# Performance work log

Measured on AMD Instinct MI355X. Metric: run time of the kernel, lower is better.

The kernel has to match this reference:

```python
import jax, jax.numpy as jnp
import numpy as np

D_MODEL = 2048
H_TOTAL = 32
D_HEAD = D_MODEL // H_TOTAL  # 64
H_ACTIVE = 4
ROPE_BASE = 10000.0


def _apply_rope(t, cos, sin):
    # t: [B, H, T, DH]; cos/sin: [T, DH//2]; interleaved pair rotation
    t1 = t[..., 0::2]
    t2 = t[..., 1::2]
    r1 = t1 * cos - t2 * sin
    r2 = t1 * sin + t2 * cos
    return jnp.stack([r1, r2], axis=-1).reshape(t.shape)


def setup_inputs() -> dict:
    key = jax.random.key(0)
    ks = jax.random.split(key, 4)
    x = jax.random.normal(ks[0], (4, 1024, D_MODEL), dtype=jnp.float32)
    w_router = jax.random.normal(ks[1], (D_MODEL, H_TOTAL), dtype=jnp.float32) * 0.02
    w_qkv = jax.random.normal(ks[2], (D_MODEL, 3 * D_MODEL), dtype=jnp.float32) * 0.02
    w_out = jax.random.normal(ks[3], (D_MODEL, D_MODEL), dtype=jnp.float32) * 0.02
    return {"x": x, "w_router": w_router, "w_qkv": w_qkv, "w_out": w_out}


def reference(x, w_router, w_qkv, w_out):
    B, T, _ = x.shape
    # --- SwitchRouter: per-token probabilities over heads ---
    probs = jax.nn.softmax(x @ w_router, axis=-1)            # [B, T, H]
    # top-h_active heads per token (dense-math equivalent of sparse dispatch)
    _, top_idx = jax.lax.top_k(probs, H_ACTIVE)              # [B, T, HA]
    mask = jnp.sum(jax.nn.one_hot(top_idx, H_TOTAL, dtype=x.dtype), axis=-2)  # [B, T, H]
    gate = probs * mask                                      # router-scored gate

    # --- QKV projection ---
    qkv = x @ w_qkv                                          # [B, T, 3D]
    q, k, v = jnp.split(qkv, 3, axis=-1)
    def to_heads(t):
        return t.reshape(B, T, H_TOTAL, D_HEAD).transpose(0, 2, 1, 3)  # [B, H, T, DH]
    q, k, v = to_heads(q), to_heads(k), to_heads(v)

    # --- RoPE ---
    inv_freq = 1.0 / (ROPE_BASE ** (jnp.arange(0, D_HEAD, 2, dtype=jnp.float32) / D_HEAD))
    ang = jnp.arange(T, dtype=jnp.float32)[:, None] * inv_freq[None, :]  # [T, DH/2]
    cos, sin = jnp.cos(ang), jnp.sin(ang)
    q = _apply_rope(q, cos, sin)
    k = _apply_rope(k, cos, sin)

    # --- causal SDPA ---
    scores = jnp.einsum('bhqd,bhkd->bhqk', q, k) / np.float32(np.sqrt(D_HEAD))
    causal = jnp.tril(jnp.ones((T, T), dtype=bool))
    scores = jnp.where(causal, scores, jnp.finfo(scores.dtype).min)
    attn = jax.nn.softmax(scores, axis=-1)
    out = jnp.einsum('bhqk,bhkd->bhqd', attn, v)             # [B, H, T, DH]

    # --- gate: only active heads contribute (scatter-back equivalent) ---
    out = out * gate.transpose(0, 2, 1)[..., None]           # [B, H, T, DH]
    out = out.transpose(0, 2, 1, 3).reshape(B, T, D_MODEL)
    return out @ w_out
```

## Files before the change

### kernel.cpp

```cpp
#include <hip/hip_runtime.h>
#include <hip/hip_bf16.h>
#include <stdint.h>
#include <stddef.h>

typedef __attribute__((ext_vector_type(8))) short bf16x8;
typedef __attribute__((ext_vector_type(8))) unsigned short u16x8;
typedef __attribute__((ext_vector_type(4))) float f32x4;
typedef __attribute__((ext_vector_type(16))) float f32x16;

#define TT 1024

__device__ __forceinline__ unsigned short f2bf(float f){
  unsigned u = __builtin_bit_cast(unsigned, f);
  unsigned r = 0x7fffu + ((u >> 16) & 1u);
  return (unsigned short)((u + r) >> 16);
}
__device__ __forceinline__ float bf2f(unsigned short s){
  unsigned u = ((unsigned)s) << 16;
  return __builtin_bit_cast(float, u);
}
__device__ __forceinline__ void gload16(const unsigned short* g, unsigned short* l){
  __builtin_amdgcn_global_load_lds(
      (const __attribute__((address_space(1))) void*)g,
      (__attribute__((address_space(3))) void*)l, 16, 0, 0);
}

#define MFMA32(a, b, c) __builtin_amdgcn_mfma_f32_32x32x16_bf16((a), (b), (c), 0, 0, 0)
#define MFMA_B16(a, b, c) __builtin_amdgcn_mfma_f32_16x16x32_bf16((a), (b), (c), 0, 0, 0)

__global__ void transpose_w_kernel(const float* __restrict__ wqkv, const float* __restrict__ wout,
                                   unsigned short* __restrict__ wqkvT, unsigned short* __restrict__ woutT){
  __shared__ float tile[32][33];
  const float* in; unsigned short* out; int C;
  int bx = blockIdx.x;
  if (bx < 192){ in = wqkv; out = wqkvT; C = 6144; }
  else         { in = wout; out = woutT; C = 2048; bx -= 192; }
  const int R = 2048;
  int c0 = bx * 32, r0 = blockIdx.y * 32;
  for (int i = threadIdx.y; i < 32; i += 8)
    tile[i][threadIdx.x] = in[(size_t)(r0 + i) * C + c0 + threadIdx.x];
  __syncthreads();
  for (int i = threadIdx.y; i < 32; i += 8)
    out[(size_t)(c0 + i) * R + r0 + threadIdx.x] = f2bf(tile[threadIdx.x][i]);
}

__global__ __launch_bounds__(256) void prep_kernel(const float* __restrict__ x,
                                                   const float* __restrict__ wr,
                                                   unsigned short* __restrict__ x_bf,
                                                   float* __restrict__ gate,
                                                   unsigned char* __restrict__ heads4,
                                                   float* __restrict__ tab){
  __shared__ float xc[8 * 256];
  __shared__ float red[8 * 8 * 32];
  const int tid = threadIdx.x;
  const int tok0 = blockIdx.x * 8;
  const int p = tid >> 5, h = tid & 31;

  if (blockIdx.x < 128){
    int i2 = blockIdx.x * 256 + tid;
    int pos = i2 >> 5, ii = i2 & 31;
    float freq = powf(10000.0f, -(float)ii / 32.0f);
    float ang = (float)pos * freq;
    tab[i2 * 2]     = cosf(ang);
    tab[i2 * 2 + 1] = sinf(ang);
  }

  float acc[8] = {0.f,0.f,0.f,0.f,0.f,0.f,0.f,0.f};
  for (int kb = 0; kb < 8; kb++){
    __syncthreads();
    {
      int tok = tid >> 5, e = (tid & 31) * 8;
      const float* xp = x + (size_t)(tok0 + tok) * 2048 + kb * 256 + e;
      float4 v0 = *(const float4*)xp, v1 = *(const float4*)(xp + 4);
      float vals[8] = {v0.x, v0.y, v0.z, v0.w, v1.x, v1.y, v1.z, v1.w};
      u16x8 ob;
      #pragma unroll
      for (int jj = 0; jj < 8; jj++) ob[jj] = f2bf(vals[jj]);
      *(u16x8*)(x_bf + (size_t)(tok0 + tok) * 2048 + kb * 256 + e) = ob;
      #pragma unroll
      for (int jj = 0; jj < 8; jj++) xc[tok * 256 + e + jj] = vals[jj];
    }
    __syncthreads();
    const float* wp = wr + (size_t)(kb * 256 + p * 32) * 32 + h;
    #pragma unroll 4
    for (int j = 0; j < 32; j++){
      float wv = wp[j * 32];
      #pragma unroll
      for (int tok = 0; tok < 8; tok++)
        acc[tok] += xc[tok * 256 + p * 32 + j] * wv;
    }
  }
  #pragma unroll
  for (int tok = 0; tok < 8; tok++) red[(p * 8 + tok) * 32 + h] = acc[tok];
  __syncthreads();
  {
    int lane = tid & 63;
    int tok = (tid >> 6) * 2 + (lane >> 5);
    int hh = lane & 31;
    float logit = 0.f;
    #pragma unroll
    for (int pp = 0; pp < 8; pp++) logit += red[(pp * 8 + tok) * 32 + hh];
    float m = logit;
    #pragma unroll
    for (int s = 16; s >= 1; s >>= 1) m = fmaxf(m, __shfl_xor(m, s));
    float e = __expf(logit - m);
    float sum = e;
    #pragma unroll
    for (int s = 16; s >= 1; s >>= 1) sum += __shfl_xor(sum, s);
    float prob = e / sum;
    float v = logit; int sel = 0;
    #pragma unroll
    for (int rr2 = 0; rr2 < 4; rr2++){
      float bv = v; int bi = hh;
      #pragma unroll
      for (int s = 16; s >= 1; s >>= 1){
        float ov = __shfl_xor(bv, s); int oi = __shfl_xor(bi, s);
        if (ov > bv || (ov == bv && oi < bi)) { bv = ov; bi = oi; }
      }
      if (hh == bi) { sel = 1; v = -3.4e38f; }
    }
    gate[(size_t)(tok0 + tok) * 32 + hh] = sel ? prob : 0.f;
    unsigned long long bal = __ballot(sel != 0);
    unsigned selmask = (unsigned)(bal >> ((lane >> 5) * 32));
    if (sel){
      int r = __popc(selmask & ((1u << hh) - 1u));
      heads4[(size_t)(tok0 + tok) * 4 + r] = (unsigned char)hh;
    }
  }
}

__global__ void compact_kernel(const unsigned char* __restrict__ heads4,
                               unsigned short* __restrict__ idx, int* __restrict__ counts){
  int bh = blockIdx.x;
  int b = bh >> 5, h = bh & 31;
  int lane = threadIdx.x;
  int base = 0;
  for (int c = 0; c < 16; c++){
    int t = c * 64 + lane;
    unsigned u = ((const unsigned*)heads4)[b * 1024 + t];
    int r = -1;
    if (((u      ) & 255) == (unsigned)h) r = 0;
    else if (((u >>  8) & 255) == (unsigned)h) r = 1;
    else if (((u >> 16) & 255) == (unsigned)h) r = 2;
    else if (((u >> 24) & 255) == (unsigned)h) r = 3;
    bool act = (r >= 0);
    unsigned long long mask = __ballot(act);
    int pos = base + __popcll(mask & ((1ull << lane) - 1ull));
    if (act) idx[bh * 1024 + pos] = (unsigned short)(t | (r << 10));
    base += __popcll(mask);
  }
  if (lane == 0) counts[bh] = base;
}

template<int MREP, int EPI>
__global__ __launch_bounds__(256, 2) void gemmk(const unsigned short* __restrict__ A,
                                                const unsigned short* __restrict__ Bt,
                                                float* __restrict__ Cf,
                                                unsigned short* __restrict__ kbuf,
                                                unsigned short* __restrict__ vt,
                                                const float* __restrict__ tab,
                                                int N, int K, int nbm){
  extern __shared__ unsigned short smem[];
  constexpr int BM = MREP * 64;
  constexpr int AU = MREP * 2048;
  constexpr int SLOT = AU + 4096;
  const int nblk = gridDim.x;
  const int raw = blockIdx.x;
  const int tile = (raw & 7) * (nblk >> 3) + (raw >> 3);
  const int bn = tile / nbm, bm = tile % nbm;

  const int tid = threadIdx.x, lane = tid & 63, wid = tid >> 6;
  const int wrow = wid >> 1, wcol = wid & 1;
  const int l31 = lane & 31, hi = lane >> 5;
  const int X = ((l31 >> 1) & 7) << 4;

  const unsigned short* gA[MREP];
  const unsigned short* gB[2];
  #pragma unroll
  for (int p = 0; p < MREP; p++){
    int L = tid * 16 + p * 4096;
    int line = L >> 7;
    int cs = (L & 127) ^ ((line & 7) << 4);
    gA[p] = A + (size_t)(bm * BM + line * 2 + (cs >> 6)) * K + ((cs & 63) >> 1);
  }
  #pragma unroll
  for (int p = 0; p < 2; p++){
    int L = tid * 16 + p * 4096;
    int line = L >> 7;
    int cs = (L & 127) ^ ((line & 7) << 4);
    gB[p] = Bt + (size_t)(bn * 128 + line * 2 + (cs >> 6)) * K + ((cs & 63) >> 1);
  }

  f32x16 acc[MREP][2];
  #pragma unroll
  for (int i = 0; i < MREP; i++)
    #pragma unroll
    for (int j = 0; j < 2; j++) acc[i][j] = f32x16{0,0,0,0,0,0,0,0,0,0,0,0,0,0,0,0};

  const int NT = K >> 5;
  #pragma unroll
  for (int tt = 0; tt < 2; tt++){
    unsigned short* sb = smem + tt * SLOT;
    #pragma unroll
    for (int p = 0; p < MREP; p++) gload16(gA[p] + (size_t)tt * 32, sb + tid * 8 + p * 2048);
    #pragma unroll
    for (int p = 0; p < 2; p++)    gload16(gB[p] + (size_t)tt * 32, sb + AU + tid * 8 + p * 2048);
  }

  for (int t = 0; t < NT; ++t){
    if (t < NT - 1){
      if constexpr (MREP == 4) asm volatile("s_waitcnt vmcnt(6)" ::: "memory");
      else                     asm volatile("s_waitcnt vmcnt(4)" ::: "memory");
    } else                     asm volatile("s_waitcnt vmcnt(0)" ::: "memory");
    __builtin_amdgcn_s_barrier();
    __builtin_amdgcn_sched_barrier(0);
    const unsigned short* bs = smem + (t % 3) * SLOT;
    unsigned short* ns = smem + ((t + 2) % 3) * SLOT;
    const bool st = (t + 2 < NT);
    #pragma unroll
    for (int ks = 0; ks < 2; ks++){
      const int bo = (((l31 & 1) * 64 + ks * 32 + hi * 16) ^ X) >> 1;
      bf16x8 av[MREP], bv[2];
      #pragma unroll
      for (int i = 0; i < MREP; i++)
        av[i] = *(const bf16x8*)(bs + (wrow * (MREP * 16) + i * 16 + (l31 >> 1)) * 64 + bo);
      #pragma unroll
      for (int j = 0; j < 2; j++)
        bv[j] = *(const bf16x8*)(bs + AU + (wcol * 32 + j * 16 + (l31 >> 1)) * 64 + bo);
      if (st){
        if (ks == 0){
          #pragma unroll
          for (int p = 0; p < MREP / 2 + 1; p++)
            gload16(gA[p] + (size_t)(t + 2) * 32, ns + tid * 8 + p * 2048);
        } else {
          #pragma unroll
          for (int p = MREP / 2 + 1; p < MREP; p++)
            gload16(gA[p] + (size_t)(t + 2) * 32, ns + tid * 8 + p * 2048);
          #pragma unroll
          for (int p = 0; p < 2; p++)
            gload16(gB[p] + (size_t)(t + 2) * 32, ns + AU + tid * 8 + p * 2048);
        }
      }
      #pragma unroll
      for (int i = 0; i < MREP; i++){
        acc[i][0] = MFMA32(av[i], bv[0], acc[i][0]);
        acc[i][1] = MFMA32(av[i], bv[1], acc[i][1]);
      }
    }
  }

  if constexpr (EPI == 1){
    if (bn < 16){
      #pragma unroll
      for (int i = 0; i < MREP; i++){
        #pragma unroll
        for (int j = 0; j < 2; j++){
          int col = bn * 128 + wcol * 64 + j * 32 + l31;
          int ii = (col & 63) >> 1;
          #pragma unroll
          for (int g = 0; g < 4; g++){
            #pragma unroll
            for (int rr = 0; rr < 4; rr++){
              int row = bm * BM + wrow * (BM / 2) + i * 32 + g * 8 + hi * 4 + rr;
              int pos = row & (TT - 1);
              const float* tp = tab + ((size_t)pos * 32 + ii) * 2;
              float c = tp[0], s = tp[1];
              float val = acc[i][j][g * 4 + rr];
              float pv = __shfl_xor(val, 1);
              float res = (lane & 1) ? (pv * s + val * c) : (val * c - pv * s);
              kbuf[(size_t)row * 2048 + col] = f2bf(res);
            }
          }
        }
      }
    } else {
      #pragma unroll
      for (int i = 0; i < MREP; i++){
        #pragma unroll
        for (int j = 0; j < 2; j++){
          int vcol = bn * 128 + wcol * 64 + j * 32 + l31 - 2048;
          int hh = vcol >> 6, d = vcol & 63;
          int row0 = bm * BM + wrow * (BM / 2) + i * 32 + hi * 4;
          int b = row0 >> 10, t0 = row0 & (TT - 1);
          #pragma unroll
          for (int g = 0; g < 4; g++){
            ushort4 pk;
            pk.x = f2bf(acc[i][j][g * 4 + 0]); pk.y = f2bf(acc[i][j][g * 4 + 1]);
            pk.z = f2bf(acc[i][j][g * 4 + 2]); pk.w = f2bf(acc[i][j][g * 4 + 3]);
            *(ushort4*)(vt + ((size_t)((b * 32 + hh) * 64 + d)) * TT + t0 + g * 8) = pk;
          }
        }
      }
    }
  } else {
    #pragma unroll
    for (int i = 0; i < MREP; i++){
      #pragma unroll
      for (int j = 0; j < 2; j++){
        int col = bn * 128 + wcol * 64 + j * 32 + l31;
        #pragma unroll
        for (int g = 0; g < 4; g++){
          #pragma unroll
          for (int rr = 0; rr < 4; rr++){
            size_t row = (size_t)(bm * BM + wrow * (BM / 2) + i * 32 + g * 8 + hi * 4 + rr);
            Cf[row * N + col] = acc[i][j][g * 4 + rr];
          }
        }
      }
    }
  }
}

__global__ __launch_bounds__(256) void attn_fused(const unsigned short* __restrict__ x_bf,
                                                  const unsigned short* __restrict__ wqkvT,
                                                  const unsigned short* __restrict__ kbuf,
                                                  const unsigned short* __restrict__ vt,
                                                  const float* __restrict__ gate,
                                                  const unsigned short* __restrict__ idx,
                                                  const int* __restrict__ counts,
                                                  const float* __restrict__ tab,
                                                  unsigned short* __restrict__ attn_out){
  __shared__ unsigned short Ks[64 * 64];
  __shared__ unsigned short Vs[64 * 64];
  __shared__ unsigned short Ps[4][16 * 64];
  __shared__ unsigned short Qb[4][16 * 64];
  const int bh = blockIdx.x, qt = blockIdx.y;
  const int count = counts[bh];
  if (qt * 64 >= count) return;
  const int b = bh >> 5, h = bh & 31;
  const int tid = threadIdx.x, lane = tid & 63, w = tid >> 6;
  const int li = lane & 15, lg = lane >> 4;
  const unsigned short* myidx = idx + bh * 1024 + qt * 64;
  const int nvalid = min(64, count - qt * 64);
  const int qmax = myidx[nvalid - 1] & 1023;

  int qi[4];
  #pragma unroll
  for (int r = 0; r < 4; r++){
    int s = w * 16 + lg * 4 + r;
    qi[r] = (s < nvalid) ? (myidx[s] & 1023) : -1;
  }

  {
    int s = w * 16 + li;
    int tokA = (s < nvalid) ? (myidx[s] & 1023) : 0;
    const unsigned short* xrow = x_bf + (size_t)(b * 1024 + tokA) * 2048;
    const unsigned short* wq = wqkvT + (size_t)(h * 64) * 2048;
    f32x4 qa[4];
    #pragma unroll
    for (int ni = 0; ni < 4; ni++) qa[ni] = f32x4{0.f, 0.f, 0.f, 0.f};
    #pragma unroll 2
    for (int kk = 0; kk < 64; kk++){
      int k0 = kk * 32 + lg * 8;
      bf16x8 af = *(const bf16x8*)(xrow + k0);
      #pragma unroll
      for (int ni = 0; ni < 4; ni++){
        bf16x8 bw = *(const bf16x8*)(wq + (size_t)(ni * 16 + li) * 2048 + k0);
        qa[ni] = MFMA_B16(af, bw, qa[ni]);
      }
    }
    #pragma unroll
    for (int ni = 0; ni < 4; ni++){
      int col = ni * 16 + li;
      #pragma unroll
      for (int r = 0; r < 4; r++){
        int tq = (qi[r] < 0) ? 0 : qi[r];
        const float* tp = tab + ((size_t)tq * 32 + (col >> 1)) * 2;
        float c = tp[0], sn = tp[1];
        float val = qa[ni][r];
        float pv = __shfl_xor(val, 1);
        float res = (li & 1) ? (pv * sn + val * c) : (val * c - pv * sn);
        int row = lg * 4 + r;
        Qb[w][(row * 128 + ((col * 2) ^ ((row & 7) << 4))) >> 1] = f2bf(res * 0.125f);
      }
    }
  }
  const int kX = (li & 7) << 4;
  bf16x8 qf0 = *(const bf16x8*)(&Qb[w][(li * 128 + ((lg * 16) ^ kX)) >> 1]);
  bf16x8 qf1 = *(const bf16x8*)(&Qb[w][(li * 128 + ((64 + lg * 16) ^ kX)) >> 1]);

  f32x4 o[4];
  #pragma unroll
  for (int i = 0; i < 4; i++) o[i] = f32x4{0.f, 0.f, 0.f, 0.f};
  float m_run[4], l_run[4];
  #pragma unroll
  for (int r = 0; r < 4; r++){ m_run[r] = -1e30f; l_run[r] = 0.f; }

  const int nkt = (qmax >> 6) + 1;
  for (int kt = 0; kt < nkt; kt++){
    const int kb = kt * 64;
    #pragma unroll
    for (int s2 = 0; s2 < 2; s2++){
      int ss = s2 * 256 + tid;
      int r = ss >> 3;
      int ce = (((ss & 7) * 16) ^ ((r & 7) << 4)) >> 1;
      gload16(kbuf + (size_t)(b * TT + kb + r) * 2048 + h * 64 + ce, &Ks[ss * 8]);
      gload16(vt + (size_t)(bh * 64 + r) * TT + kb + ce, &Vs[ss * 8]);
    }
    __syncthreads();

    f32x4 s4[4];
    #pragma unroll
    for (int ni = 0; ni < 4; ni++){
      int rb = (ni * 16 + li) * 128;
      bf16x8 k0 = *(const bf16x8*)(&Ks[(rb + ((lg * 16) ^ kX)) >> 1]);
      bf16x8 k1 = *(const bf16x8*)(&Ks[(rb + ((64 + lg * 16) ^ kX)) >> 1]);
      f32x4 t = f32x4{0.f, 0.f, 0.f, 0.f};
      t = MFMA_B16(qf0, k0, t);
      t = MFMA_B16(qf1, k1, t);
      s4[ni] = t;
    }
    float mt[4];
    #pragma unroll
    for (int r = 0; r < 4; r++) mt[r] = -1e30f;
    #pragma unroll
    for (int ni = 0; ni < 4; ni++){
      int kidx = kb + ni * 16 + li;
      #pragma unroll
      for (int r = 0; r < 4; r++){
        float val = s4[ni][r];
        val = (kidx <= qi[r]) ? val : -1e30f;
        s4[ni][r] = val;
        mt[r] = fmaxf(mt[r], val);
      }
    }
    #pragma unroll
    for (int r = 0; r < 4; r++){
      #pragma unroll
      for (int sh = 8; sh >= 1; sh >>= 1) mt[r] = fmaxf(mt[r], __shfl_xor(mt[r], sh));
      float mnew = fmaxf(m_run[r], mt[r]);
      float corr = __expf(m_run[r] - mnew);
      m_run[r] = mnew;
      l_run[r] *= corr;
      #pragma unroll
      for (int j = 0; j < 4; j++) o[j][r] *= corr;
    }
    float rs[4] = {0.f, 0.f, 0.f, 0.f};
    #pragma unroll
    for (int ni = 0; ni < 4; ni++)
      #pragma unroll
      for (int r = 0; r < 4; r++){
        float p = __expf(s4[ni][r] - m_run[r]);
        s4[ni][r] = p;
        rs[r] += p;
      }
    #pragma unroll
    for (int r = 0; r < 4; r++){
      #pragma unroll
      for (int sh = 8; sh >= 1; sh >>= 1) rs[r] += __shfl_xor(rs[r], sh);
      l_run[r] += rs[r];
    }
    #pragma unroll
    for (int ni = 0; ni < 4; ni++)
      #pragma unroll
      for (int r = 0; r < 4; r++){
        int row = lg * 4 + r;
        Ps[w][(row * 128 + (((ni * 16 + li) * 2) ^ ((row & 7) << 4))) >> 1] = f2bf(s4[ni][r]);
      }
    #pragma unroll
    for (int ks = 0; ks < 2; ks++){
      bf16x8 pa = *(const bf16x8*)(&Ps[w][(li * 128 + ((ks * 64 + lg * 16) ^ kX)) >> 1]);
      #pragma unroll
      for (int ni = 0; ni < 4; ni++){
        bf16x8 vb = *(const bf16x8*)(&Vs[((ni * 16 + li) * 128 + ((ks * 64 + lg * 16) ^ kX)) >> 1]);
        o[ni] = MFMA_B16(pa, vb, o[ni]);
      }
    }
    __syncthreads();
  }
  #pragma unroll
  for (int r = 0; r < 4; r++){
    if (qi[r] < 0) continue;
    float g = gate[(size_t)(b * TT + qi[r]) * 32 + h];
    float inv = g / l_run[r];
    #pragma unroll
    for (int ni = 0; ni < 4; ni++)
      attn_out[(size_t)(b * TT + qi[r]) * 2048 + h * 64 + ni * 16 + li] = f2bf(o[ni][r] * inv);
  }
}

extern "C" void kernel_launch(void* const* d_in, const int* in_sizes, int n_in,
                              void* d_out, int out_size, void* d_ws, size_t ws_size,
                              hipStream_t stream){
  const float* x        = (const float*)d_in[0];
  const float* w_router = (const float*)d_in[1];
  const float* w_qkv    = (const float*)d_in[2];
  const float* w_out    = (const float*)d_in[3];
  float* out = (float*)d_out;
  char* ws = (char*)d_ws;

  unsigned short* kbuf   = (unsigned short*)(ws);
  unsigned short* vt     = (unsigned short*)(ws + 16777216);
  unsigned short* idx    = (unsigned short*)(ws + 37748736);
  int* counts            = (int*)(ws + 38010880);
  unsigned char* heads4  = (unsigned char*)(ws + 38011392);
  unsigned short* x_bf   = (unsigned short*)(ws + 50331648);
  unsigned short* wqkvT  = (unsigned short*)(ws + 67108864);
  unsigned short* woutT  = (unsigned short*)(ws + 92274688);
  float* gate            = (float*)(ws + 100663296);
  float* tab             = (float*)(ws + 101187584);
  unsigned short* attn   = (unsigned short*)(ws + 67108864 + 8388608);

  constexpr int KV_LDS  = 3 * (4 * 4096 + 8192);
  constexpr int OUT_LDS = 3 * (2 * 4096 + 8192);
  (void)hipFuncSetAttribute(reinterpret_cast<const void*>(&gemmk<4, 1>),
                            hipFuncAttributeMaxDynamicSharedMemorySize, KV_LDS);
  (void)hipFuncSetAttribute(reinterpret_cast<const void*>(&gemmk<2, 0>),
                            hipFuncAttributeMaxDynamicSharedMemorySize, OUT_LDS);

  hipLaunchKernelGGL(transpose_w_kernel, dim3(256, 64), dim3(32, 8), 0, stream, w_qkv, w_out, wqkvT, woutT);
  hipLaunchKernelGGL(prep_kernel, dim3(512), dim3(256), 0, stream, x, w_router, x_bf, gate, heads4, tab);
  hipLaunchKernelGGL(compact_kernel, dim3(128), dim3(64), 0, stream, heads4, idx, counts);
  hipLaunchKernelGGL((gemmk<4, 1>), dim3(512), dim3(256), KV_LDS, stream,
                     x_bf, wqkvT + (size_t)2048 * 2048, (float*)nullptr, kbuf, vt, tab, 4096, 2048, 16);
  (void)hipMemsetAsync(attn, 0, (size_t)4096 * 2048 * 2, stream);
  hipLaunchKernelGGL(attn_fused, dim3(128, 16), dim3(256), 0, stream,
                     x_bf, wqkvT, kbuf, vt, gate, idx, counts, tab, attn);
  hipLaunchKernelGGL((gemmk<2, 0>), dim3(512), dim3(256), OUT_LDS, stream,
                     attn, woutT, out, (unsigned short*)nullptr, (unsigned short*)nullptr,
                     (const float*)nullptr, 2048, 2048, 32);
}
```

Before: 297.8 us.

## Split sparse Q projection into separate split-K GEMM kernel before attention

Moves the per-token Q projection and RoPE out of the attention kernel into a dedicated qgemm kernel. That kernel computes a 64-token by 64-dim tile per block, splits K across four waves, reduces the partial sums in LDS and writes RoPE'd bf16 Q into a compact per-(token, slot) buffer. The attention kernel then just loads Q fragments, applies the 1/8 scale to the scores, and drops the XOR swizzle on its K, V and P LDS tiles, which may add bank conflicts. The attention output buffer now reuses the x_bf region. This adds a kernel launch and a global round trip for Q, in exchange for better MFMA reuse in the projection.

```diff
diff --git a/kernel.cpp b/kernel.cpp
--- a/kernel.cpp
+++ b/kernel.cpp
@@ -150,6 +150,80 @@
     base += __popcll(mask);
   }
   if (lane == 0) counts[bh] = base;
+}
+
+__global__ __launch_bounds__(256) void qgemm_kernel(const unsigned short* __restrict__ x_bf,
+                                                    const unsigned short* __restrict__ wqkvT,
+                                                    const unsigned short* __restrict__ idx,
+                                                    const int* __restrict__ counts,
+                                                    const float* __restrict__ tab,
+                                                    unsigned short* __restrict__ qact){
+  __shared__ float red[4][64][64];
+  const int bh = blockIdx.x, qt = blockIdx.y;
+  const int count = counts[bh];
+  if (qt * 64 >= count) return;
+  const int b = bh >> 5, h = bh & 31;
+  const int tid = threadIdx.x, lane = tid & 63, w = tid >> 6;
+  const int li = lane & 15, lg = lane >> 4;
+  const int nvalid = min(64, count - qt * 64);
+  const unsigned short* myidx = idx + bh * 1024 + qt * 64;
+
+  int atok[4];
+  #pragma unroll
+  for (int ai = 0; ai < 4; ai++){
+    int s = ai * 16 + li;
+    atok[ai] = (s < nvalid) ? (myidx[s] & 1023) : 0;
+  }
+  const unsigned short* Bbase = wqkvT + (size_t)(h * 64) * 2048;
+
+  f32x4 acc[4][4];
+  #pragma unroll
+  for (int i = 0; i < 4; i++)
+    #pragma unroll
+    for (int j = 0; j < 4; j++) acc[i][j] = f32x4{0.f, 0.f, 0.f, 0.f};
+
+  const int k0w = w * 512;
+  #pragma unroll 2
+  for (int ks = 0; ks < 16; ks++){
+    int k0 = k0w + ks * 32 + lg * 8;
+    bf16x8 af[4], bw[4];
+    #pragma unroll
+    for (int ai = 0; ai < 4; ai++)
+      af[ai] = *(const bf16x8*)(x_bf + (size_t)(b * 1024 + atok[ai]) * 2048 + k0);
+    #pragma unroll
+    for (int ni = 0; ni < 4; ni++)
+      bw[ni] = *(const bf16x8*)(Bbase + (size_t)(ni * 16 + li) * 2048 + k0);
+    #pragma unroll
+    for (int ai = 0; ai < 4; ai++)
+      #pragma unroll
+      for (int ni = 0; ni < 4; ni++)
+        acc[ai][ni] = MFMA_B16(af[ai], bw[ni], acc[ai][ni]);
+  }
+  #pragma unroll
+  for (int ai = 0; ai < 4; ai++)
+    #pragma unroll
+    for (int ni = 0; ni < 4; ni++)
+      #pragma unroll
+      for (int rr = 0; rr < 4; rr++)
+        red[w][ai * 16 + lg * 4 + rr][ni * 16 + li] = acc[ai][ni][rr];
+  __syncthreads();
+
+  int q = tid >> 2, dbase = (tid & 3) * 16;
+  if (q < nvalid){
+    int e = myidx[q];
+    int tok = e & 1023, r = e >> 10;
+    unsigned short* op = qact + ((size_t)((b << 10) + tok) * 4 + r) * 64;
+    const float* tp = tab + ((size_t)tok * 32 + (dbase >> 1)) * 2;
+    #pragma unroll
+    for (int p = 0; p < 8; p++){
+      int d0 = dbase + 2 * p;
+      float v0 = red[0][q][d0] + red[1][q][d0] + red[2][q][d0] + red[3][q][d0];
+      float v1 = red[0][q][d0 + 1] + red[1][q][d0 + 1] + red[2][q][d0 + 1] + red[3][q][d0 + 1];
+      float c = tp[2 * p], s = tp[2 * p + 1];
+      op[d0]     = f2bf(v0 * c - v1 * s);
+      op[d0 + 1] = f2bf(v0 * s + v1 * c);
+    }
+  }
 }
 
 template<int MREP, int EPI>
@@ -311,19 +385,16 @@
   }
 }
 
-__global__ __launch_bounds__(256) void attn_fused(const unsigned short* __restrict__ x_bf,
-                                                  const unsigned short* __restrict__ wqkvT,
-                                                  const unsigned short* __restrict__ kbuf,
-                                                  const unsigned short* __restrict__ vt,
-                                                  const float* __restrict__ gate,
-                                                  const unsigned short* __restrict__ idx,
-                                                  const int* __restrict__ counts,
-                                                  const float* __restrict__ tab,
-                                                  unsigned short* __restrict__ attn_out){
+__global__ __launch_bounds__(256) void attn_sparse_kernel(const unsigned short* __restrict__ qact,
+                                                          const unsigned short* __restrict__ kbuf,
+                                                          const unsigned short* __restrict__ vt,
+                                                          const float* __restrict__ gate,
+                                                          const unsigned short* __restrict__ idx,
+                                                          const int* __restrict__ counts,
+                                                          unsigned short* __restrict__ attn_out){
   __shared__ unsigned short Ks[64 * 64];
   __shared__ unsigned short Vs[64 * 64];
   __shared__ unsigned short Ps[4][16 * 64];
-  __shared__ unsigned short Qb[4][16 * 64];
   const int bh = blockIdx.x, qt = blockIdx.y;
   const int count = counts[bh];
   if (qt * 64 >= count) return;
@@ -340,45 +411,14 @@
     int s = w * 16 + lg * 4 + r;
     qi[r] = (s < nvalid) ? (myidx[s] & 1023) : -1;
   }
-
+  bf16x8 qf0, qf1;
   {
     int s = w * 16 + li;
-    int tokA = (s < nvalid) ? (myidx[s] & 1023) : 0;
-    const unsigned short* xrow = x_bf + (size_t)(b * 1024 + tokA) * 2048;
-    const unsigned short* wq = wqkvT + (size_t)(h * 64) * 2048;
-    f32x4 qa[4];
-    #pragma unroll
-    for (int ni = 0; ni < 4; ni++) qa[ni] = f32x4{0.f, 0.f, 0.f, 0.f};
-    #pragma unroll 2
-    for (int kk = 0; kk < 64; kk++){
-      int k0 = kk * 32 + lg * 8;
-      bf16x8 af = *(const bf16x8*)(xrow + k0);
-      #pragma unroll
-      for (int ni = 0; ni < 4; ni++){
-        bf16x8 bw = *(const bf16x8*)(wq + (size_t)(ni * 16 + li) * 2048 + k0);
-        qa[ni] = MFMA_B16(af, bw, qa[ni]);
-      }
-    }
-    #pragma unroll
-    for (int ni = 0; ni < 4; ni++){
-      int col = ni * 16 + li;
-      #pragma unroll
-      for (int r = 0; r < 4; r++){
-        int tq = (qi[r] < 0) ? 0 : qi[r];
-        const float* tp = tab + ((size_t)tq * 32 + (col >> 1)) * 2;
-        float c = tp[0], sn = tp[1];
-        float val = qa[ni][r];
-        float pv = __shfl_xor(val, 1);
-        float res = (li & 1) ? (pv * sn + val * c) : (val * c - pv * sn);
-        int row = lg * 4 + r;
-        Qb[w][(row * 128 + ((col * 2) ^ ((row & 7) << 4))) >> 1] = f2bf(res * 0.125f);
-      }
-    }
-  }
-  const int kX = (li & 7) << 4;
-  bf16x8 qf0 = *(const bf16x8*)(&Qb[w][(li * 128 + ((lg * 16) ^ kX)) >> 1]);
-  bf16x8 qf1 = *(const bf16x8*)(&Qb[w][(li * 128 + ((64 + lg * 16) ^ kX)) >> 1]);
-
+    int e2 = (s < nvalid) ? myidx[s] : 0;
+    const unsigned short* qp = qact + ((size_t)((b << 10) + (e2 & 1023)) * 4 + (e2 >> 10)) * 64;
+    qf0 = *(const bf16x8*)(qp + lg * 8);
+    qf1 = *(const bf16x8*)(qp + 32 + lg * 8);
+  }
   f32x4 o[4];
   #pragma unroll
   for (int i = 0; i < 4; i++) o[i] = f32x4{0.f, 0.f, 0.f, 0.f};
@@ -391,20 +431,18 @@
     const int kb = kt * 64;
     #pragma unroll
     for (int s2 = 0; s2 < 2; s2++){
-      int ss = s2 * 256 + tid;
-      int r = ss >> 3;
-      int ce = (((ss & 7) * 16) ^ ((r & 7) << 4)) >> 1;
-      gload16(kbuf + (size_t)(b * TT + kb + r) * 2048 + h * 64 + ce, &Ks[ss * 8]);
-      gload16(vt + (size_t)(bh * 64 + r) * TT + kb + ce, &Vs[ss * 8]);
+      int s = s2 * 256 + tid;
+      int r = s >> 3, c = (s & 7) * 8;
+      gload16(kbuf + (size_t)(b * TT + kb + r) * 2048 + h * 64 + c, &Ks[s * 8]);
+      gload16(vt + (size_t)(bh * 64 + r) * TT + kb + c, &Vs[s * 8]);
     }
     __syncthreads();
 
     f32x4 s4[4];
     #pragma unroll
     for (int ni = 0; ni < 4; ni++){
-      int rb = (ni * 16 + li) * 128;
-      bf16x8 k0 = *(const bf16x8*)(&Ks[(rb + ((lg * 16) ^ kX)) >> 1]);
-      bf16x8 k1 = *(const bf16x8*)(&Ks[(rb + ((64 + lg * 16) ^ kX)) >> 1]);
+      bf16x8 k0 = *(const bf16x8*)(&Ks[(ni * 16 + li) * 64 + lg * 8]);
+      bf16x8 k1 = *(const bf16x8*)(&Ks[(ni * 16 + li) * 64 + 32 + lg * 8]);
       f32x4 t = f32x4{0.f, 0.f, 0.f, 0.f};
       t = MFMA_B16(qf0, k0, t);
       t = MFMA_B16(qf1, k1, t);
@@ -418,7 +456,7 @@
       int kidx = kb + ni * 16 + li;
       #pragma unroll
       for (int r = 0; r < 4; r++){
-        float val = s4[ni][r];
+        float val = s4[ni][r] * 0.125f;
         val = (kidx <= qi[r]) ? val : -1e30f;
         s4[ni][r] = val;
         mt[r] = fmaxf(mt[r], val);
@@ -453,16 +491,14 @@
     #pragma unroll
     for (int ni = 0; ni < 4; ni++)
       #pragma unroll
-      for (int r = 0; r < 4; r++){
-        int row = lg * 4 + r;
-        Ps[w][(row * 128 + (((ni * 16 + li) * 2) ^ ((row & 7) << 4))) >> 1] = f2bf(s4[ni][r]);
-      }
+      for (int r = 0; r < 4; r++)
+        Ps[w][(lg * 4 + r) * 64 + ni * 16 + li] = f2bf(s4[ni][r]);
     #pragma unroll
     for (int ks = 0; ks < 2; ks++){
-      bf16x8 pa = *(const bf16x8*)(&Ps[w][(li * 128 + ((ks * 64 + lg * 16) ^ kX)) >> 1]);
+      bf16x8 pa = *(const bf16x8*)(&Ps[w][li * 64 + ks * 32 + lg * 8]);
       #pragma unroll
       for (int ni = 0; ni < 4; ni++){
-        bf16x8 vb = *(const bf16x8*)(&Vs[((ni * 16 + li) * 128 + ((ks * 64 + lg * 16) ^ kX)) >> 1]);
+        bf16x8 vb = *(const bf16x8*)(&Vs[(ni * 16 + li) * 64 + ks * 32 + lg * 8]);
         o[ni] = MFMA_B16(pa, vb, o[ni]);
       }
     }
@@ -491,6 +527,7 @@
 
   unsigned short* kbuf   = (unsigned short*)(ws);
   unsigned short* vt     = (unsigned short*)(ws + 16777216);
+  unsigned short* qact   = (unsigned short*)(ws + 33554432);
   unsigned short* idx    = (unsigned short*)(ws + 37748736);
   int* counts            = (int*)(ws + 38010880);
   unsigned char* heads4  = (unsigned char*)(ws + 38011392);
@@ -499,10 +536,10 @@
   unsigned short* woutT  = (unsigned short*)(ws + 92274688);
   float* gate            = (float*)(ws + 100663296);
   float* tab             = (float*)(ws + 101187584);
-  unsigned short* attn   = (unsigned short*)(ws + 67108864 + 8388608);
-
-  constexpr int KV_LDS  = 3 * (4 * 4096 + 8192);
-  constexpr int OUT_LDS = 3 * (2 * 4096 + 8192);
+  unsigned short* attn   = x_bf;
+
+  constexpr int KV_LDS  = 3 * (4 * 4096 + 8192) * 2 / 2;
+  constexpr int OUT_LDS = 3 * (2 * 4096 + 8192) * 2 / 2;
   (void)hipFuncSetAttribute(reinterpret_cast<const void*>(&gemmk<4, 1>),
                             hipFuncAttributeMaxDynamicSharedMemorySize, KV_LDS);
   (void)hipFuncSetAttribute(reinterpret_cast<const void*>(&gemmk<2, 0>),
@@ -513,9 +550,11 @@
   hipLaunchKernelGGL(compact_kernel, dim3(128), dim3(64), 0, stream, heads4, idx, counts);
   hipLaunchKernelGGL((gemmk<4, 1>), dim3(512), dim3(256), KV_LDS, stream,
                      x_bf, wqkvT + (size_t)2048 * 2048, (float*)nullptr, kbuf, vt, tab, 4096, 2048, 16);
+  hipLaunchKernelGGL(qgemm_kernel, dim3(128, 16), dim3(256), 0, stream,
+                     x_bf, wqkvT, idx, counts, tab, qact);
   (void)hipMemsetAsync(attn, 0, (size_t)4096 * 2048 * 2, stream);
-  hipLaunchKernelGGL(attn_fused, dim3(128, 16), dim3(256), 0, stream,
-                     x_bf, wqkvT, kbuf, vt, gate, idx, counts, tab, attn);
+  hipLaunchKernelGGL(attn_sparse_kernel, dim3(128, 16), dim3(256), 0, stream,
+                     qact, kbuf, vt, gate, idx, counts, attn);
   hipLaunchKernelGGL((gemmk<2, 0>), dim3(512), dim3(256), OUT_LDS, stream,
                      attn, woutT, out, (unsigned short*)nullptr, (unsigned short*)nullptr,
                      (const float*)nullptr, 2048, 2048, 32);
```

New measurement: 267.0 us. -10.3%, faster.
